# Optimization experiments

Measured on AMD Instinct MI355X. Metric: run time of the kernel, lower is better.

The kernel has to match this reference:

```python
import jax, jax.numpy as jnp
import numpy as np

N_CONV = 3
FEAT = 128
N_RBF = 20
CUTOFF = 5.0
EPS = 1e-15
N_NODES = 10000
N_EDGES = 160000


def setup_inputs() -> dict:
    key = jax.random.key(0)
    ks = jax.random.split(key, 8)
    N, E = N_NODES, N_EDGES
    cg_xyz = jax.random.normal(ks[0], (N, 3), jnp.float32) * 2.0
    # Directed, self-loop-free edge list (both i<j and i>j present, so the
    # original make_directed() is a no-op on this data).
    src = jax.random.randint(ks[1], (E,), 0, N)
    off = jax.random.randint(ks[2], (E,), 1, N)
    CG_nbr_list = jnp.stack([src, (src + off) % N], axis=1)
    cg_s = jax.random.normal(ks[3], (N, FEAT), jnp.float32)
    s = 1.0 / np.sqrt(FEAT)
    # Per-conv-layer weights of ENMessageBlock: inv_dense = Dense(F->F, silu) + Dense(F->3F);
    # dist_embed = ExpNormalBasis(n_rbf) -> Dense(n_rbf->3F) * cosine envelope.
    W1 = jax.random.normal(ks[4], (N_CONV, FEAT, FEAT), jnp.float32) * s
    b1 = jnp.zeros((N_CONV, FEAT), jnp.float32)
    W2 = jax.random.normal(ks[5], (N_CONV, FEAT, 3 * FEAT), jnp.float32) * s
    b2 = jnp.zeros((N_CONV, 3 * FEAT), jnp.float32)
    Wr = jax.random.normal(ks[6], (N_CONV, N_RBF, 3 * FEAT), jnp.float32) / np.sqrt(N_RBF)
    br = jnp.zeros((N_CONV, 3 * FEAT), jnp.float32)
    return {"cg_xyz": cg_xyz, "CG_nbr_list": CG_nbr_list, "cg_s": cg_s,
            "W1": W1, "b1": b1, "W2": W2, "b2": b2, "Wr": Wr, "br": br}


def _expnorm_rbf(dist):
    # ExpNormalBasis: exp(-beta * (exp(-d) - mu)^2), mu in [exp(-cutoff), 1]
    mu = jnp.linspace(np.exp(-CUTOFF), 1.0, N_RBF, dtype=jnp.float32)
    beta = np.float32((2.0 / N_RBF * (1.0 - np.exp(-CUTOFF))) ** -2)
    return jnp.exp(-beta * (jnp.exp(-dist)[:, None] - mu) ** 2)  # (E, n_rbf)


def _cos_envelope(dist):
    return jnp.where(dist < CUTOFF, 0.5 * (jnp.cos(jnp.pi * dist / CUTOFF) + 1.0), 0.0)


def reference(cg_xyz, CG_nbr_list, cg_s, W1, b1, W2, b2, Wr, br):
    N = cg_s.shape[0]
    i, j = CG_nbr_list[:, 0], CG_nbr_list[:, 1]
    r_ij = cg_xyz[j] - cg_xyz[i]                      # (E, 3)
    dist = jnp.sqrt((r_ij ** 2 + EPS).sum(-1))        # (E,)
    unit = r_ij / dist[:, None]                        # (E, 3)
    rbf = _expnorm_rbf(dist)                           # (E, n_rbf) edge-invariant across layers
    env = _cos_envelope(dist)[:, None]                 # (E, 1)

    s_i = cg_s                                         # (N, F)
    v_i = jnp.zeros((N, FEAT, 3), cg_s.dtype)          # (N, F, 3)
    for l in range(N_CONV):
        phi = jax.nn.silu(s_i @ W1[l] + b1[l]) @ W2[l] + b2[l]   # (N, 3F)
        w_s = (rbf @ Wr[l] + br[l]) * env                         # (E, 3F)
        prod = phi[j] * w_s                                       # (E, 3F) gather + gate
        ds = prod[:, :FEAT]                                       # scalar message
        gate_v = prod[:, FEAT:2 * FEAT]                           # gates v_j
        gate_u = prod[:, 2 * FEAT:]                               # gates unit vector
        dv_ij = gate_u[:, :, None] * unit[:, None, :] + gate_v[:, :, None] * v_i[j]  # (E, F, 3)
        s_i = s_i + jax.ops.segment_sum(ds, i, num_segments=N)
        v_i = v_i + jax.ops.segment_sum(dv_ij, i, num_segments=N)
    return s_i, v_i
```

## Files before the change

kernel.cpp:

```cpp
#include <hip/hip_runtime.h>
#include <hip/hip_bf16.h>

#define NRBF 20
#define KAUG 24

typedef __attribute__((ext_vector_type(8))) short short8;
typedef __attribute__((ext_vector_type(4))) float float4v;
typedef __attribute__((ext_vector_type(2))) _Float16 half2v;
typedef unsigned short ushort_t;

__device__ __forceinline__ float bf2f(ushort_t u) {
    return __uint_as_float(((unsigned)u) << 16);
}
__device__ __forceinline__ ushort_t f2bf(float f) {
    unsigned u = __float_as_uint(f);
    u += 0x7FFF + ((u >> 16) & 1);
    return (ushort_t)(u >> 16);
}
__device__ __forceinline__ float ldin(const void* p, size_t idx, int isbf) {
    return isbf ? bf2f(((const ushort_t*)p)[idx]) : ((const float*)p)[idx];
}
__device__ __forceinline__ void stout(void* p, size_t idx, float v, int isbf) {
    if (isbf) ((ushort_t*)p)[idx] = f2bf(v);
    else      ((float*)p)[idx] = v;
}
__device__ __forceinline__ float dot2(half2v a, half2v b, float c) {
#if __has_builtin(__builtin_amdgcn_fdot2)
    return __builtin_amdgcn_fdot2(a, b, c, false);
#else
    return c + (float)a.x * (float)b.x + (float)a.y * (float)b.y;
#endif
}

union F4H {
    float4v f;
    half2v  h[4];
};

__global__ void detect_kernel(const void* __restrict__ xyz, int* __restrict__ flag,
                              int* __restrict__ deg, int N) {
    int idx = blockIdx.x * blockDim.x + threadIdx.x;
    if (idx < N) deg[idx] = 0;
    if (blockIdx.x == 0 && threadIdx.x < 64) {
        const ushort_t* u = (const ushort_t*)xyz;
        unsigned e0 = (u[2 * threadIdx.x] >> 7) & 0xFF;
        unsigned long long bad = __ballot(e0 >= 0x90);
        if (threadIdx.x == 0) *flag = (__popcll(bad) > 2) ? 0 : 1;
    }
}

__global__ void prelude_kernel(const void* __restrict__ xyz, const int* __restrict__ nbr,
                               const void* __restrict__ cg_s,
                               const void* __restrict__ W1, const void* __restrict__ W2,
                               const void* __restrict__ Wr, const void* __restrict__ br,
                               float* __restrict__ s_acc, ushort_t* __restrict__ s_hi,
                               ushort_t* __restrict__ s_lo, int* __restrict__ deg,
                               ushort_t* __restrict__ B1hi, ushort_t* __restrict__ B1lo,
                               ushort_t* __restrict__ B2hi, ushort_t* __restrict__ B2lo,
                               _Float16* __restrict__ WrT,
                               int N128, int E, const int* __restrict__ flagp) {
    int isbf = *flagp;
    int idx = blockIdx.x * blockDim.x + threadIdx.x;
    if (idx < E) {
        int i = nbr[2 * idx], j = nbr[2 * idx + 1];
        float dx = ldin(xyz, 3 * j,     isbf) - ldin(xyz, 3 * i,     isbf);
        float dy = ldin(xyz, 3 * j + 1, isbf) - ldin(xyz, 3 * i + 1, isbf);
        float dz = ldin(xyz, 3 * j + 2, isbf) - ldin(xyz, 3 * i + 2, isbf);
        float dist = sqrtf(dx * dx + dy * dy + dz * dz + 3e-15f);
        if (dist < 5.0f) atomicAdd(&deg[i], 1);
    }
    if (idx < N128) {
        float v = ldin(cg_s, idx, isbf);
        s_acc[idx] = v;
        ushort_t hi = f2bf(v);
        s_hi[idx] = hi;
        s_lo[idx] = f2bf(v - bf2f(hi));
    }
    const int NW1 = 3 * 4 * 8 * 64;
    const int NW2 = 3 * 4 * 24 * 64;
    const int NWT = 3 * 384;
    if (idx < NW1) {
        int lane = idx & 63;
        int t = idx >> 6;
        int nt = t % 8; t /= 8;
        int ks = t % 4; int l = t / 4;
        int n = lane & 15, quad = lane >> 4;
        int col = nt * 16 + n;
        size_t base = (size_t)l * 128 * 128;
        size_t fo = (size_t)idx * 8;
        #pragma unroll
        for (int j = 0; j < 8; j++) {
            int k = ks * 32 + quad * 8 + j;
            float v = ldin(W1, base + (size_t)k * 128 + col, isbf);
            ushort_t hi = f2bf(v);
            B1hi[fo + j] = hi;
            B1lo[fo + j] = f2bf(v - bf2f(hi));
        }
    } else if (idx < NW1 + NW2) {
        int i2 = idx - NW1;
        int lane = i2 & 63;
        int t = i2 >> 6;
        int nt = t % 24; t /= 24;
        int ks = t % 4; int l = t / 4;
        int n = lane & 15, quad = lane >> 4;
        int col = nt * 16 + n;
        size_t base = (size_t)l * 128 * 384;
        size_t fo = (size_t)i2 * 8;
        #pragma unroll
        for (int j = 0; j < 8; j++) {
            int k = ks * 32 + quad * 8 + j;
            float v = ldin(W2, base + (size_t)k * 384 + col, isbf);
            ushort_t hi = f2bf(v);
            B2hi[fo + j] = hi;
            B2lo[fo + j] = f2bf(v - bf2f(hi));
        }
    } else if (idx < NW1 + NW2 + NWT) {
        int i2 = idx - NW1 - NW2;
        int l = i2 / 384, col = i2 % 384;
        _Float16* wt = WrT + ((size_t)l * 384 + col) * KAUG;
        #pragma unroll
        for (int k = 0; k < KAUG; k++) {
            float v = 0.f;
            if (k < NRBF) v = ldin(Wr, ((size_t)l * NRBF + k) * 384 + col, isbf);
            else if (k == NRBF) v = ldin(br, (size_t)l * 384 + col, isbf);
            wt[k] = (_Float16)v;
        }
    }
}

__global__ void scan_kernel(int* __restrict__ deg, int* __restrict__ rowptr, int N) {
    __shared__ int part[256];
    int t = threadIdx.x;
    int chunk = (N + 255) / 256;
    int lo = t * chunk, hi = min(lo + chunk, N);
    int s = 0;
    for (int i = lo; i < hi; i++) s += deg[i];
    part[t] = s;
    __syncthreads();
    for (int off = 1; off < 256; off <<= 1) {
        int v = (t >= off) ? part[t - off] : 0;
        __syncthreads();
        if (t >= off) part[t] += v;
        __syncthreads();
    }
    int base = (t == 0) ? 0 : part[t - 1];
    for (int i = lo; i < hi; i++) {
        rowptr[i] = base;
        int d = deg[i];
        deg[i] = base;
        base += d;
    }
    if (t == 0) rowptr[N] = part[255];
}

__global__ void pack_kernel(const void* __restrict__ xyz, const int* __restrict__ nbr,
                            int* __restrict__ cursor, int* __restrict__ jlist,
                            float4* __restrict__ upos, _Float16* __restrict__ rbfh,
                            int E, const int* __restrict__ flagp) {
    int isbf = *flagp;
    int e = blockIdx.x * blockDim.x + threadIdx.x;
    if (e >= E) return;
    int i = nbr[2 * e], j = nbr[2 * e + 1];
    float dx = ldin(xyz, 3 * j,     isbf) - ldin(xyz, 3 * i,     isbf);
    float dy = ldin(xyz, 3 * j + 1, isbf) - ldin(xyz, 3 * i + 1, isbf);
    float dz = ldin(xyz, 3 * j + 2, isbf) - ldin(xyz, 3 * i + 2, isbf);
    float dist = sqrtf(dx * dx + dy * dy + dz * dz + 3e-15f);
    if (!(dist < 5.0f)) return;
    constexpr float PI = 3.14159265358979323846f;
    float ev = 0.5f * (cosf(PI * dist * 0.2f) + 1.0f);
    int pos = atomicAdd(&cursor[i], 1);
    jlist[pos] = j;
    float inv = 1.0f / dist;
    upos[pos] = make_float4(dx * inv, dy * inv, dz * inv, ev);
    constexpr double EM5 = 0.006737946999085467;
    constexpr float MU0 = (float)EM5;
    constexpr float DMU = (float)((1.0 - EM5) / 19.0);
    constexpr float BETA = (float)(1.0 / ((0.1 * (1.0 - EM5)) * (0.1 * (1.0 - EM5))));
    float ed = expf(-dist);
    _Float16* rp = rbfh + (size_t)pos * KAUG;
    #pragma unroll
    for (int k = 0; k < NRBF; k++) {
        float dmu = ed - (MU0 + k * DMU);
        rp[k] = (_Float16)(ev * expf(-BETA * dmu * dmu));
    }
    rp[NRBF] = (_Float16)ev;
    #pragma unroll
    for (int k = NRBF + 1; k < KAUG; k++) rp[k] = (_Float16)0.f;
}

template <int ACT, int OUTMODE, int NTILES>
__global__ __launch_bounds__(256) void mfma_gemm(
    const ushort_t* __restrict__ Ahi, const ushort_t* __restrict__ Alo,
    const ushort_t* __restrict__ Bhi, const ushort_t* __restrict__ Blo,
    const void* __restrict__ bias, size_t biasoff,
    ushort_t* __restrict__ out_hi, ushort_t* __restrict__ out_lo,
    int M, const int* __restrict__ flagp) {
    constexpr int Ncols = NTILES * 16;
    int isbf = *flagp;
    int nt = blockIdx.x % NTILES;
    int bx = blockIdx.x / NTILES;
    int tid = threadIdx.x;
    int wave = tid >> 6, lane = tid & 63;
    int m = lane & 15, quad = lane >> 4;
    int brow = bx * 64 + wave * 16;
    int row = brow + m;
    float4v acc = {};
    short8 zero8 = {};
    #pragma unroll
    for (int ks = 0; ks < 4; ks++) {
        short8 ah = zero8, al = zero8;
        if (row < M) {
            size_t ao = (size_t)row * 128 + ks * 32 + quad * 8;
            ah = *reinterpret_cast<const short8*>(Ahi + ao);
            al = *reinterpret_cast<const short8*>(Alo + ao);
        }
        size_t fo = (((size_t)ks * NTILES + nt) * 64 + lane) * 8;
        short8 bh = *reinterpret_cast<const short8*>(Bhi + fo);
        acc = __builtin_amdgcn_mfma_f32_16x16x32_bf16(ah, bh, acc, 0, 0, 0);
        acc = __builtin_amdgcn_mfma_f32_16x16x32_bf16(al, bh, acc, 0, 0, 0);
        if (!isbf) {
            short8 bl = *reinterpret_cast<const short8*>(Blo + fo);
            acc = __builtin_amdgcn_mfma_f32_16x16x32_bf16(ah, bl, acc, 0, 0, 0);
        }
    }
    int col = nt * 16 + m;
    float bv = ldin(bias, biasoff + col, isbf);
    #pragma unroll
    for (int r = 0; r < 4; r++) {
        int orow = brow + quad * 4 + r;
        if (orow >= M) continue;
        float x = acc[r] + bv;
        if (ACT) x = x / (1.0f + expf(-x));
        size_t oo = (size_t)orow * Ncols + col;
        ushort_t h = f2bf(x);
        out_hi[oo] = h;
        if (OUTMODE == 0) out_lo[oo] = f2bf(x - bf2f(h));
    }
}

template <int L0, int LAST>
__global__ __launch_bounds__(128, 8) void node_kernel(
    const int* __restrict__ rowptr, const int* __restrict__ jlist,
    const float4* __restrict__ upos, const _Float16* __restrict__ rbfh,
    const _Float16* __restrict__ WrT,
    const ushort_t* __restrict__ phi,
    const float* __restrict__ v_old, const ushort_t* __restrict__ vh_old,
    float* __restrict__ s_acc, ushort_t* __restrict__ s_hi, ushort_t* __restrict__ s_lo,
    float* __restrict__ v_new, ushort_t* __restrict__ vh_new,
    void* __restrict__ out, int N, const int* __restrict__ flagp) {
    int isbf = *flagp;
    int tt = threadIdx.x;
    int node = blockIdx.x;

    F4H wc0[3], wc1[3], wc2[3];
    {
        const float4v* w0p = (const float4v*)(WrT + (size_t)tt * KAUG);
        const float4v* w1p = (const float4v*)(WrT + (size_t)(tt + 128) * KAUG);
        const float4v* w2p = (const float4v*)(WrT + (size_t)(tt + 256) * KAUG);
        #pragma unroll
        for (int r = 0; r < 3; r++) {
            wc0[r].f = w0p[r]; wc1[r].f = w1p[r]; wc2[r].f = w2p[r];
        }
    }
    int start = __builtin_amdgcn_readfirstlane(rowptr[node]);
    int end   = __builtin_amdgcn_readfirstlane(rowptr[node + 1]);

    float dsv = 0.f, ax = 0.f, ay = 0.f, az = 0.f;
    int j = (start < end) ? __builtin_amdgcn_readfirstlane(jlist[start]) : 0;
    for (int k = start; k < end; k++) {
        int jn = j;
        if (k + 1 < end) jn = __builtin_amdgcn_readfirstlane(jlist[k + 1]);
        float4 u4 = upos[k];
        const float4v* rp4 = (const float4v*)(rbfh + (size_t)k * KAUG);
        F4H rv0, rv1, rv2;
        rv0.f = rp4[0]; rv1.f = rp4[1]; rv2.f = rp4[2];
        float w0 = 0.f, w1 = 0.f, w2 = 0.f;
        #pragma unroll
        for (int q = 0; q < 4; q++) {
            w0 = dot2(rv0.h[q], wc0[0].h[q], w0);
            w1 = dot2(rv0.h[q], wc1[0].h[q], w1);
            w2 = dot2(rv0.h[q], wc2[0].h[q], w2);
        }
        #pragma unroll
        for (int q = 0; q < 4; q++) {
            w0 = dot2(rv1.h[q], wc0[1].h[q], w0);
            w1 = dot2(rv1.h[q], wc1[1].h[q], w1);
            w2 = dot2(rv1.h[q], wc2[1].h[q], w2);
        }
        #pragma unroll
        for (int q = 0; q < 4; q++) {
            w0 = dot2(rv2.h[q], wc0[2].h[q], w0);
            w1 = dot2(rv2.h[q], wc1[2].h[q], w1);
            w2 = dot2(rv2.h[q], wc2[2].h[q], w2);
        }
        size_t jb = (size_t)j * 384;
        dsv += bf2f(phi[jb + tt]) * w0;
        float gv = bf2f(phi[jb + 128 + tt]) * w1;
        float gu = bf2f(phi[jb + 256 + tt]) * w2;
        if (L0) {
            ax += gu * u4.x; ay += gu * u4.y; az += gu * u4.z;
        } else {
            const ushort_t* vj = &vh_old[jb + (size_t)tt * 3];
            ax += gu * u4.x + gv * bf2f(vj[0]);
            ay += gu * u4.y + gv * bf2f(vj[1]);
            az += gu * u4.z + gv * bf2f(vj[2]);
        }
        j = jn;
    }
    size_t so = (size_t)node * 128 + tt;
    float snew = s_acc[so] + dsv;
    size_t ib = (size_t)node * 384 + (size_t)tt * 3;
    float vx = L0 ? ax : v_old[ib]     + ax;
    float vy = L0 ? ay : v_old[ib + 1] + ay;
    float vz = L0 ? az : v_old[ib + 2] + az;
    if (LAST) {
        stout(out, so, snew, isbf);
        size_t ob = (size_t)N * 128 + ib;
        stout(out, ob,     vx, isbf);
        stout(out, ob + 1, vy, isbf);
        stout(out, ob + 2, vz, isbf);
    } else {
        s_acc[so] = snew;
        ushort_t hi = f2bf(snew);
        s_hi[so] = hi;
        s_lo[so] = f2bf(snew - bf2f(hi));
        v_new[ib] = vx; v_new[ib + 1] = vy; v_new[ib + 2] = vz;
        vh_new[ib]     = f2bf(vx);
        vh_new[ib + 1] = f2bf(vy);
        vh_new[ib + 2] = f2bf(vz);
    }
}

extern "C" void kernel_launch(void* const* d_in, const int* in_sizes, int n_in,
                              void* d_out, int out_size, void* d_ws, size_t ws_size,
                              hipStream_t stream) {
    const int N = in_sizes[0] / 3;
    const int E = in_sizes[1] / 2;
    const void* xyz  = d_in[0];
    const int*  nbr  = (const int*)d_in[1];
    const void* cg_s = d_in[2];
    const void* W1   = d_in[3];
    const void* b1   = d_in[4];
    const void* W2   = d_in[5];
    const void* b2   = d_in[6];
    const void* Wr   = d_in[7];
    const void* br   = d_in[8];

    size_t off = 0;
    auto alloc = [&](size_t bytes) -> char* {
        char* p = (char*)d_ws + off;
        off = (off + bytes + 63) & ~(size_t)63;
        return p;
    };
    int*       flag   = (int*)alloc(64);
    float*     s_acc  = (float*)alloc((size_t)N * 128 * 4);
    float*     vA     = (float*)alloc((size_t)N * 384 * 4);
    float*     vB     = (float*)alloc((size_t)N * 384 * 4);
    int*       rowptr = (int*)alloc((size_t)(N + 1) * 4);
    int*       deg    = (int*)alloc((size_t)N * 4);
    int*       jlist  = (int*)alloc((size_t)E * 4);
    float4*    upos   = (float4*)alloc((size_t)(E + 16) * 16);
    _Float16*  rbfh   = (_Float16*)alloc((size_t)(E + 16) * KAUG * 2);
    _Float16*  WrT    = (_Float16*)alloc((size_t)3 * 384 * KAUG * 2);
    ushort_t*  s_hi   = (ushort_t*)alloc((size_t)N * 128 * 2);
    ushort_t*  s_lo   = (ushort_t*)alloc((size_t)N * 128 * 2);
    ushort_t*  h_hi   = (ushort_t*)alloc((size_t)N * 128 * 2);
    ushort_t*  h_lo   = (ushort_t*)alloc((size_t)N * 128 * 2);
    ushort_t*  phi    = (ushort_t*)alloc((size_t)N * 384 * 2);
    ushort_t*  vhA    = (ushort_t*)alloc((size_t)N * 384 * 2);
    ushort_t*  vhB    = (ushort_t*)alloc((size_t)N * 384 * 2);
    ushort_t*  B1hi   = (ushort_t*)alloc((size_t)3 * 4 * 8 * 64 * 8 * 2);
    ushort_t*  B1lo   = (ushort_t*)alloc((size_t)3 * 4 * 8 * 64 * 8 * 2);
    ushort_t*  B2hi   = (ushort_t*)alloc((size_t)3 * 4 * 24 * 64 * 8 * 2);
    ushort_t*  B2lo   = (ushort_t*)alloc((size_t)3 * 4 * 24 * 64 * 8 * 2);

    detect_kernel<<<(N + 255) / 256, 256, 0, stream>>>(xyz, flag, deg, N);
    const int N128 = N * 128;
    const int pg = (max(E, N128) + 255) / 256;
    prelude_kernel<<<pg, 256, 0, stream>>>(xyz, nbr, cg_s, W1, W2, Wr, br,
                                           s_acc, s_hi, s_lo, deg,
                                           B1hi, B1lo, B2hi, B2lo, WrT,
                                           N128, E, flag);
    scan_kernel<<<1, 256, 0, stream>>>(deg, rowptr, N);
    pack_kernel<<<(E + 255) / 256, 256, 0, stream>>>(xyz, nbr, deg, jlist, upos,
                                                     rbfh, E, flag);

    const int gx = (N + 63) / 64;
    for (int l = 0; l < 3; l++) {
        mfma_gemm<1, 0, 8><<<gx * 8, 256, 0, stream>>>(
            s_hi, s_lo,
            B1hi + (size_t)l * 4 * 8 * 64 * 8, B1lo + (size_t)l * 4 * 8 * 64 * 8,
            b1, (size_t)l * 128, h_hi, h_lo, N, flag);
        mfma_gemm<0, 1, 24><<<gx * 24, 256, 0, stream>>>(
            h_hi, h_lo,
            B2hi + (size_t)l * 4 * 24 * 64 * 8, B2lo + (size_t)l * 4 * 24 * 64 * 8,
            b2, (size_t)l * 384, phi, (ushort_t*)nullptr, N, flag);
        const _Float16* wrt = WrT + (size_t)l * 384 * KAUG;
        if (l == 0) {
            node_kernel<1, 0><<<N, 128, 0, stream>>>(
                rowptr, jlist, upos, rbfh, wrt, phi,
                vA, vhA, s_acc, s_hi, s_lo, vA, vhA, d_out, N, flag);
        } else if (l == 1) {
            node_kernel<0, 0><<<N, 128, 0, stream>>>(
                rowptr, jlist, upos, rbfh, wrt, phi,
                vA, vhA, s_acc, s_hi, s_lo, vB, vhB, d_out, N, flag);
        } else {
            node_kernel<0, 1><<<N, 128, 0, stream>>>(
                rowptr, jlist, upos, rbfh, wrt, phi,
                vB, vhB, s_acc, s_hi, s_lo, vB, vhB, d_out, N, flag);
        }
    }
}
```

Measured before the change: 329.9 us.

## Fuse all stages into one persistent cooperative kernel with grid syncs

```diff
diff --git a/kernel.cpp b/kernel.cpp
--- a/kernel.cpp
+++ b/kernel.cpp
@@ -1,5 +1,8 @@
 #include <hip/hip_runtime.h>
 #include <hip/hip_bf16.h>
+#include <hip/hip_cooperative_groups.h>
+
+namespace cg = cooperative_groups;
 
 #define NRBF 20
 #define KAUG 24
@@ -37,104 +40,111 @@
     half2v  h[4];
 };
 
-__global__ void detect_kernel(const void* __restrict__ xyz, int* __restrict__ flag,
-                              int* __restrict__ deg, int N) {
-    int idx = blockIdx.x * blockDim.x + threadIdx.x;
-    if (idx < N) deg[idx] = 0;
-    if (blockIdx.x == 0 && threadIdx.x < 64) {
-        const ushort_t* u = (const ushort_t*)xyz;
-        unsigned e0 = (u[2 * threadIdx.x] >> 7) & 0xFF;
+struct KParams {
+    const void* xyz; const int* nbr; const void* cg_s;
+    const void* W1;  const void* b1; const void* W2; const void* b2;
+    const void* Wr;  const void* br;
+    int* flag; float* s_acc; float* vA; float* vB;
+    int* rowptr; int* deg; int* jlist; float4* upos;
+    _Float16* rbfh; _Float16* WrT;
+    ushort_t* s_hi; ushort_t* s_lo; ushort_t* h_hi; ushort_t* h_lo;
+    ushort_t* phi;  ushort_t* vhA;  ushort_t* vhB;
+    ushort_t* B1hi; ushort_t* B1lo; ushort_t* B2hi; ushort_t* B2lo;
+    void* out; int N, E, gx;
+};
+
+__device__ __forceinline__ void phase_detect(const KParams& p) {
+    int tid = threadIdx.x;
+    for (int idx = blockIdx.x * 256 + tid; idx < p.N; idx += gridDim.x * 256)
+        p.deg[idx] = 0;
+    if (blockIdx.x == 0 && tid < 64) {
+        const ushort_t* u = (const ushort_t*)p.xyz;
+        unsigned e0 = (u[2 * tid] >> 7) & 0xFF;
         unsigned long long bad = __ballot(e0 >= 0x90);
-        if (threadIdx.x == 0) *flag = (__popcll(bad) > 2) ? 0 : 1;
-    }
-}
-
-__global__ void prelude_kernel(const void* __restrict__ xyz, const int* __restrict__ nbr,
-                               const void* __restrict__ cg_s,
-                               const void* __restrict__ W1, const void* __restrict__ W2,
-                               const void* __restrict__ Wr, const void* __restrict__ br,
-                               float* __restrict__ s_acc, ushort_t* __restrict__ s_hi,
-                               ushort_t* __restrict__ s_lo, int* __restrict__ deg,
-                               ushort_t* __restrict__ B1hi, ushort_t* __restrict__ B1lo,
-                               ushort_t* __restrict__ B2hi, ushort_t* __restrict__ B2lo,
-                               _Float16* __restrict__ WrT,
-                               int N128, int E, const int* __restrict__ flagp) {
-    int isbf = *flagp;
-    int idx = blockIdx.x * blockDim.x + threadIdx.x;
-    if (idx < E) {
-        int i = nbr[2 * idx], j = nbr[2 * idx + 1];
-        float dx = ldin(xyz, 3 * j,     isbf) - ldin(xyz, 3 * i,     isbf);
-        float dy = ldin(xyz, 3 * j + 1, isbf) - ldin(xyz, 3 * i + 1, isbf);
-        float dz = ldin(xyz, 3 * j + 2, isbf) - ldin(xyz, 3 * i + 2, isbf);
-        float dist = sqrtf(dx * dx + dy * dy + dz * dz + 3e-15f);
-        if (dist < 5.0f) atomicAdd(&deg[i], 1);
-    }
-    if (idx < N128) {
-        float v = ldin(cg_s, idx, isbf);
-        s_acc[idx] = v;
-        ushort_t hi = f2bf(v);
-        s_hi[idx] = hi;
-        s_lo[idx] = f2bf(v - bf2f(hi));
-    }
+        if (tid == 0) *p.flag = (__popcll(bad) > 2) ? 0 : 1;
+    }
+}
+
+__device__ void phase_prelude(const KParams& p, int isbf) {
+    const int N128 = p.N * 128;
     const int NW1 = 3 * 4 * 8 * 64;
     const int NW2 = 3 * 4 * 24 * 64;
     const int NWT = 3 * 384;
-    if (idx < NW1) {
-        int lane = idx & 63;
-        int t = idx >> 6;
-        int nt = t % 8; t /= 8;
-        int ks = t % 4; int l = t / 4;
-        int n = lane & 15, quad = lane >> 4;
-        int col = nt * 16 + n;
-        size_t base = (size_t)l * 128 * 128;
-        size_t fo = (size_t)idx * 8;
-        #pragma unroll
-        for (int j = 0; j < 8; j++) {
-            int k = ks * 32 + quad * 8 + j;
-            float v = ldin(W1, base + (size_t)k * 128 + col, isbf);
+    int tot = (N128 > p.E) ? N128 : p.E;
+    for (int idx = blockIdx.x * 256 + threadIdx.x; idx < tot; idx += gridDim.x * 256) {
+        if (idx < p.E) {
+            int i = p.nbr[2 * idx], j = p.nbr[2 * idx + 1];
+            float dx = ldin(p.xyz, 3 * j,     isbf) - ldin(p.xyz, 3 * i,     isbf);
+            float dy = ldin(p.xyz, 3 * j + 1, isbf) - ldin(p.xyz, 3 * i + 1, isbf);
+            float dz = ldin(p.xyz, 3 * j + 2, isbf) - ldin(p.xyz, 3 * i + 2, isbf);
+            float dist = sqrtf(dx * dx + dy * dy + dz * dz + 3e-15f);
+            if (dist < 5.0f) atomicAdd(&p.deg[i], 1);
+        }
+        if (idx < N128) {
+            float v = ldin(p.cg_s, idx, isbf);
+            p.s_acc[idx] = v;
             ushort_t hi = f2bf(v);
-            B1hi[fo + j] = hi;
-            B1lo[fo + j] = f2bf(v - bf2f(hi));
-        }
-    } else if (idx < NW1 + NW2) {
-        int i2 = idx - NW1;
-        int lane = i2 & 63;
-        int t = i2 >> 6;
-        int nt = t % 24; t /= 24;
-        int ks = t % 4; int l = t / 4;
-        int n = lane & 15, quad = lane >> 4;
-        int col = nt * 16 + n;
-        size_t base = (size_t)l * 128 * 384;
-        size_t fo = (size_t)i2 * 8;
-        #pragma unroll
-        for (int j = 0; j < 8; j++) {
-            int k = ks * 32 + quad * 8 + j;
-            float v = ldin(W2, base + (size_t)k * 384 + col, isbf);
-            ushort_t hi = f2bf(v);
-            B2hi[fo + j] = hi;
-            B2lo[fo + j] = f2bf(v - bf2f(hi));
-        }
-    } else if (idx < NW1 + NW2 + NWT) {
-        int i2 = idx - NW1 - NW2;
-        int l = i2 / 384, col = i2 % 384;
-        _Float16* wt = WrT + ((size_t)l * 384 + col) * KAUG;
-        #pragma unroll
-        for (int k = 0; k < KAUG; k++) {
-            float v = 0.f;
-            if (k < NRBF) v = ldin(Wr, ((size_t)l * NRBF + k) * 384 + col, isbf);
-            else if (k == NRBF) v = ldin(br, (size_t)l * 384 + col, isbf);
-            wt[k] = (_Float16)v;
-        }
-    }
-}
-
-__global__ void scan_kernel(int* __restrict__ deg, int* __restrict__ rowptr, int N) {
+            p.s_hi[idx] = hi;
+            p.s_lo[idx] = f2bf(v - bf2f(hi));
+        }
+        if (idx < NW1) {
+            int lane = idx & 63;
+            int t = idx >> 6;
+            int nt = t % 8; t /= 8;
+            int ks = t % 4; int l = t / 4;
+            int n = lane & 15, quad = lane >> 4;
+            int col = nt * 16 + n;
+            size_t base = (size_t)l * 128 * 128;
+            size_t fo = (size_t)idx * 8;
+            #pragma unroll
+            for (int j = 0; j < 8; j++) {
+                int k = ks * 32 + quad * 8 + j;
+                float v = ldin(p.W1, base + (size_t)k * 128 + col, isbf);
+                ushort_t hi = f2bf(v);
+                p.B1hi[fo + j] = hi;
+                p.B1lo[fo + j] = f2bf(v - bf2f(hi));
+            }
+        } else if (idx < NW1 + NW2) {
+            int i2 = idx - NW1;
+            int lane = i2 & 63;
+            int t = i2 >> 6;
+            int nt = t % 24; t /= 24;
+            int ks = t % 4; int l = t / 4;
+            int n = lane & 15, quad = lane >> 4;
+            int col = nt * 16 + n;
+            size_t base = (size_t)l * 128 * 384;
+            size_t fo = (size_t)i2 * 8;
+            #pragma unroll
+            for (int j = 0; j < 8; j++) {
+                int k = ks * 32 + quad * 8 + j;
+                float v = ldin(p.W2, base + (size_t)k * 384 + col, isbf);
+                ushort_t hi = f2bf(v);
+                p.B2hi[fo + j] = hi;
+                p.B2lo[fo + j] = f2bf(v - bf2f(hi));
+            }
+        } else if (idx < NW1 + NW2 + NWT) {
+            int i2 = idx - NW1 - NW2;
+            int l = i2 / 384, col = i2 % 384;
+            _Float16* wt = p.WrT + ((size_t)l * 384 + col) * KAUG;
+            #pragma unroll
+            for (int k = 0; k < KAUG; k++) {
+                float v = 0.f;
+                if (k < NRBF) v = ldin(p.Wr, ((size_t)l * NRBF + k) * 384 + col, isbf);
+                else if (k == NRBF) v = ldin(p.br, (size_t)l * 384 + col, isbf);
+                wt[k] = (_Float16)v;
+            }
+        }
+    }
+}
+
+__device__ void scan_block(const KParams& p) {
     __shared__ int part[256];
     int t = threadIdx.x;
+    int N = p.N;
     int chunk = (N + 255) / 256;
     int lo = t * chunk, hi = min(lo + chunk, N);
     int s = 0;
-    for (int i = lo; i < hi; i++) s += deg[i];
+    for (int i = lo; i < hi; i++) s += p.deg[i];
     part[t] = s;
     __syncthreads();
     for (int off = 1; off < 256; off <<= 1) {
@@ -145,39 +155,34 @@
     }
     int base = (t == 0) ? 0 : part[t - 1];
     for (int i = lo; i < hi; i++) {
-        rowptr[i] = base;
-        int d = deg[i];
-        deg[i] = base;
+        p.rowptr[i] = base;
+        int d = p.deg[i];
+        p.deg[i] = base;
         base += d;
     }
-    if (t == 0) rowptr[N] = part[255];
-}
-
-__global__ void pack_kernel(const void* __restrict__ xyz, const int* __restrict__ nbr,
-                            int* __restrict__ cursor, int* __restrict__ jlist,
-                            float4* __restrict__ upos, _Float16* __restrict__ rbfh,
-                            int E, const int* __restrict__ flagp) {
-    int isbf = *flagp;
-    int e = blockIdx.x * blockDim.x + threadIdx.x;
-    if (e >= E) return;
-    int i = nbr[2 * e], j = nbr[2 * e + 1];
-    float dx = ldin(xyz, 3 * j,     isbf) - ldin(xyz, 3 * i,     isbf);
-    float dy = ldin(xyz, 3 * j + 1, isbf) - ldin(xyz, 3 * i + 1, isbf);
-    float dz = ldin(xyz, 3 * j + 2, isbf) - ldin(xyz, 3 * i + 2, isbf);
+    if (t == 0) p.rowptr[N] = part[255];
+}
+
+__device__ void pack_edge(const KParams& p, int isbf, int e) {
+    if (e >= p.E) return;
+    int i = p.nbr[2 * e], j = p.nbr[2 * e + 1];
+    float dx = ldin(p.xyz, 3 * j,     isbf) - ldin(p.xyz, 3 * i,     isbf);
+    float dy = ldin(p.xyz, 3 * j + 1, isbf) - ldin(p.xyz, 3 * i + 1, isbf);
+    float dz = ldin(p.xyz, 3 * j + 2, isbf) - ldin(p.xyz, 3 * i + 2, isbf);
     float dist = sqrtf(dx * dx + dy * dy + dz * dz + 3e-15f);
     if (!(dist < 5.0f)) return;
     constexpr float PI = 3.14159265358979323846f;
     float ev = 0.5f * (cosf(PI * dist * 0.2f) + 1.0f);
-    int pos = atomicAdd(&cursor[i], 1);
-    jlist[pos] = j;
+    int pos = atomicAdd(&p.deg[i], 1);
+    p.jlist[pos] = j;
     float inv = 1.0f / dist;
-    upos[pos] = make_float4(dx * inv, dy * inv, dz * inv, ev);
+    p.upos[pos] = make_float4(dx * inv, dy * inv, dz * inv, ev);
     constexpr double EM5 = 0.006737946999085467;
     constexpr float MU0 = (float)EM5;
     constexpr float DMU = (float)((1.0 - EM5) / 19.0);
     constexpr float BETA = (float)(1.0 / ((0.1 * (1.0 - EM5)) * (0.1 * (1.0 - EM5))));
     float ed = expf(-dist);
-    _Float16* rp = rbfh + (size_t)pos * KAUG;
+    _Float16* rp = p.rbfh + (size_t)pos * KAUG;
     #pragma unroll
     for (int k = 0; k < NRBF; k++) {
         float dmu = ed - (MU0 + k * DMU);
@@ -189,16 +194,15 @@
 }
 
 template <int ACT, int OUTMODE, int NTILES>
-__global__ __launch_bounds__(256) void mfma_gemm(
-    const ushort_t* __restrict__ Ahi, const ushort_t* __restrict__ Alo,
+__device__ __forceinline__ void gemm_item(
+    int item, const ushort_t* __restrict__ Ahi, const ushort_t* __restrict__ Alo,
     const ushort_t* __restrict__ Bhi, const ushort_t* __restrict__ Blo,
     const void* __restrict__ bias, size_t biasoff,
     ushort_t* __restrict__ out_hi, ushort_t* __restrict__ out_lo,
-    int M, const int* __restrict__ flagp) {
+    int M, int isbf) {
     constexpr int Ncols = NTILES * 16;
-    int isbf = *flagp;
-    int nt = blockIdx.x % NTILES;
-    int bx = blockIdx.x / NTILES;
+    int nt = item % NTILES;
+    int bx = item / NTILES;
     int tid = threadIdx.x;
     int wave = tid >> 6, lane = tid & 63;
     int m = lane & 15, quad = lane >> 4;
@@ -238,97 +242,159 @@
     }
 }
 
+__device__ void phase_g1(const KParams& p, int isbf, int l, bool withScan) {
+    const ushort_t* Bh = p.B1hi + (size_t)l * 4 * 8 * 64 * 8;
+    const ushort_t* Bl = p.B1lo + (size_t)l * 4 * 8 * 64 * 8;
+    size_t boff = (size_t)l * 128;
+    int g1 = p.gx * 8;
+    int items = g1 + (withScan ? 1 : 0);
+    for (int it = blockIdx.x; it < items; it += gridDim.x) {
+        if (withScan) {
+            if (it == 0) { scan_block(p); continue; }
+            gemm_item<1, 0, 8>(it - 1, p.s_hi, p.s_lo, Bh, Bl, p.b1, boff,
+                               p.h_hi, p.h_lo, p.N, isbf);
+        } else {
+            gemm_item<1, 0, 8>(it, p.s_hi, p.s_lo, Bh, Bl, p.b1, boff,
+                               p.h_hi, p.h_lo, p.N, isbf);
+        }
+    }
+}
+
+__device__ void phase_g2(const KParams& p, int isbf, int l, bool withPack) {
+    const ushort_t* Bh = p.B2hi + (size_t)l * 4 * 24 * 64 * 8;
+    const ushort_t* Bl = p.B2lo + (size_t)l * 4 * 24 * 64 * 8;
+    size_t boff = (size_t)l * 384;
+    int g2 = p.gx * 24;
+    int packItems = withPack ? (p.E + 255) / 256 : 0;
+    int items = g2 + packItems;
+    for (int it = blockIdx.x; it < items; it += gridDim.x) {
+        if (it < g2) {
+            gemm_item<0, 1, 24>(it, p.h_hi, p.h_lo, Bh, Bl, p.b2, boff,
+                                p.phi, (ushort_t*)nullptr, p.N, isbf);
+        } else {
+            pack_edge(p, isbf, (it - g2) * 256 + threadIdx.x);
+        }
+    }
+}
+
 template <int L0, int LAST>
-__global__ __launch_bounds__(128, 8) void node_kernel(
-    const int* __restrict__ rowptr, const int* __restrict__ jlist,
-    const float4* __restrict__ upos, const _Float16* __restrict__ rbfh,
-    const _Float16* __restrict__ WrT,
-    const ushort_t* __restrict__ phi,
-    const float* __restrict__ v_old, const ushort_t* __restrict__ vh_old,
-    float* __restrict__ s_acc, ushort_t* __restrict__ s_hi, ushort_t* __restrict__ s_lo,
-    float* __restrict__ v_new, ushort_t* __restrict__ vh_new,
-    void* __restrict__ out, int N, const int* __restrict__ flagp) {
-    int isbf = *flagp;
-    int tt = threadIdx.x;
-    int node = blockIdx.x;
+__device__ void phase_node(const KParams& p, int isbf, const _Float16* WrTl,
+                           const float* v_old, const ushort_t* vh_old,
+                           float* v_new, ushort_t* vh_new) {
+    int tid = threadIdx.x;
+    int half = tid >> 7;
+    int tt = tid & 127;
 
     F4H wc0[3], wc1[3], wc2[3];
     {
-        const float4v* w0p = (const float4v*)(WrT + (size_t)tt * KAUG);
-        const float4v* w1p = (const float4v*)(WrT + (size_t)(tt + 128) * KAUG);
-        const float4v* w2p = (const float4v*)(WrT + (size_t)(tt + 256) * KAUG);
+        const float4v* w0p = (const float4v*)(WrTl + (size_t)tt * KAUG);
+        const float4v* w1p = (const float4v*)(WrTl + (size_t)(tt + 128) * KAUG);
+        const float4v* w2p = (const float4v*)(WrTl + (size_t)(tt + 256) * KAUG);
         #pragma unroll
         for (int r = 0; r < 3; r++) {
             wc0[r].f = w0p[r]; wc1[r].f = w1p[r]; wc2[r].f = w2p[r];
         }
     }
-    int start = __builtin_amdgcn_readfirstlane(rowptr[node]);
-    int end   = __builtin_amdgcn_readfirstlane(rowptr[node + 1]);
-
-    float dsv = 0.f, ax = 0.f, ay = 0.f, az = 0.f;
-    int j = (start < end) ? __builtin_amdgcn_readfirstlane(jlist[start]) : 0;
-    for (int k = start; k < end; k++) {
-        int jn = j;
-        if (k + 1 < end) jn = __builtin_amdgcn_readfirstlane(jlist[k + 1]);
-        float4 u4 = upos[k];
-        const float4v* rp4 = (const float4v*)(rbfh + (size_t)k * KAUG);
-        F4H rv0, rv1, rv2;
-        rv0.f = rp4[0]; rv1.f = rp4[1]; rv2.f = rp4[2];
-        float w0 = 0.f, w1 = 0.f, w2 = 0.f;
-        #pragma unroll
-        for (int q = 0; q < 4; q++) {
-            w0 = dot2(rv0.h[q], wc0[0].h[q], w0);
-            w1 = dot2(rv0.h[q], wc1[0].h[q], w1);
-            w2 = dot2(rv0.h[q], wc2[0].h[q], w2);
-        }
-        #pragma unroll
-        for (int q = 0; q < 4; q++) {
-            w0 = dot2(rv1.h[q], wc0[1].h[q], w0);
-            w1 = dot2(rv1.h[q], wc1[1].h[q], w1);
-            w2 = dot2(rv1.h[q], wc2[1].h[q], w2);
-        }
-        #pragma unroll
-        for (int q = 0; q < 4; q++) {
-            w0 = dot2(rv2.h[q], wc0[2].h[q], w0);
-            w1 = dot2(rv2.h[q], wc1[2].h[q], w1);
-            w2 = dot2(rv2.h[q], wc2[2].h[q], w2);
-        }
-        size_t jb = (size_t)j * 384;
-        dsv += bf2f(phi[jb + tt]) * w0;
-        float gv = bf2f(phi[jb + 128 + tt]) * w1;
-        float gu = bf2f(phi[jb + 256 + tt]) * w2;
-        if (L0) {
-            ax += gu * u4.x; ay += gu * u4.y; az += gu * u4.z;
+    int items = (p.N + 1) >> 1;
+    for (int it = blockIdx.x; it < items; it += gridDim.x) {
+        int node = it * 2 + half;
+        if (node >= p.N) continue;
+        int start = __builtin_amdgcn_readfirstlane(p.rowptr[node]);
+        int end   = __builtin_amdgcn_readfirstlane(p.rowptr[node + 1]);
+
+        float dsv = 0.f, ax = 0.f, ay = 0.f, az = 0.f;
+        int j = (start < end) ? __builtin_amdgcn_readfirstlane(p.jlist[start]) : 0;
+        for (int k = start; k < end; k++) {
+            int jn = j;
+            if (k + 1 < end) jn = __builtin_amdgcn_readfirstlane(p.jlist[k + 1]);
+            float4 u4 = p.upos[k];
+            const float4v* rp4 = (const float4v*)(p.rbfh + (size_t)k * KAUG);
+            F4H rv0, rv1, rv2;
+            rv0.f = rp4[0]; rv1.f = rp4[1]; rv2.f = rp4[2];
+            float w0 = 0.f, w1 = 0.f, w2 = 0.f;
+            #pragma unroll
+            for (int q = 0; q < 4; q++) {
+                w0 = dot2(rv0.h[q], wc0[0].h[q], w0);
+                w1 = dot2(rv0.h[q], wc1[0].h[q], w1);
+                w2 = dot2(rv0.h[q], wc2[0].h[q], w2);
+            }
+            #pragma unroll
+            for (int q = 0; q < 4; q++) {
+                w0 = dot2(rv1.h[q], wc0[1].h[q], w0);
+                w1 = dot2(rv1.h[q], wc1[1].h[q], w1);
+                w2 = dot2(rv1.h[q], wc2[1].h[q], w2);
+            }
+            #pragma unroll
+            for (int q = 0; q < 4; q++) {
+                w0 = dot2(rv2.h[q], wc0[2].h[q], w0);
+                w1 = dot2(rv2.h[q], wc1[2].h[q], w1);
+                w2 = dot2(rv2.h[q], wc2[2].h[q], w2);
+            }
+            size_t jb = (size_t)j * 384;
+            dsv += bf2f(p.phi[jb + tt]) * w0;
+            float gv = bf2f(p.phi[jb + 128 + tt]) * w1;
+            float gu = bf2f(p.phi[jb + 256 + tt]) * w2;
+            if (L0) {
+                ax += gu * u4.x; ay += gu * u4.y; az += gu * u4.z;
+            } else {
+                const ushort_t* vj = &vh_old[jb + (size_t)tt * 3];
+                ax += gu * u4.x + gv * bf2f(vj[0]);
+                ay += gu * u4.y + gv * bf2f(vj[1]);
+                az += gu * u4.z + gv * bf2f(vj[2]);
+            }
+            j = jn;
+        }
+        size_t so = (size_t)node * 128 + tt;
+        float snew = p.s_acc[so] + dsv;
+        size_t ib = (size_t)node * 384 + (size_t)tt * 3;
+        float vx = L0 ? ax : v_old[ib]     + ax;
+        float vy = L0 ? ay : v_old[ib + 1] + ay;
+        float vz = L0 ? az : v_old[ib + 2] + az;
+        if (LAST) {
+            stout(p.out, so, snew, isbf);
+            size_t ob = (size_t)p.N * 128 + ib;
+            stout(p.out, ob,     vx, isbf);
+            stout(p.out, ob + 1, vy, isbf);
+            stout(p.out, ob + 2, vz, isbf);
         } else {
-            const ushort_t* vj = &vh_old[jb + (size_t)tt * 3];
-            ax += gu * u4.x + gv * bf2f(vj[0]);
-            ay += gu * u4.y + gv * bf2f(vj[1]);
-            az += gu * u4.z + gv * bf2f(vj[2]);
-        }
-        j = jn;
-    }
-    size_t so = (size_t)node * 128 + tt;
-    float snew = s_acc[so] + dsv;
-    size_t ib = (size_t)node * 384 + (size_t)tt * 3;
-    float vx = L0 ? ax : v_old[ib]     + ax;
-    float vy = L0 ? ay : v_old[ib + 1] + ay;
-    float vz = L0 ? az : v_old[ib + 2] + az;
-    if (LAST) {
-        stout(out, so, snew, isbf);
-        size_t ob = (size_t)N * 128 + ib;
-        stout(out, ob,     vx, isbf);
-        stout(out, ob + 1, vy, isbf);
-        stout(out, ob + 2, vz, isbf);
-    } else {
-        s_acc[so] = snew;
-        ushort_t hi = f2bf(snew);
-        s_hi[so] = hi;
-        s_lo[so] = f2bf(snew - bf2f(hi));
-        v_new[ib] = vx; v_new[ib + 1] = vy; v_new[ib + 2] = vz;
-        vh_new[ib]     = f2bf(vx);
-        vh_new[ib + 1] = f2bf(vy);
-        vh_new[ib + 2] = f2bf(vz);
-    }
+            p.s_acc[so] = snew;
+            ushort_t hi = f2bf(snew);
+            p.s_hi[so] = hi;
+            p.s_lo[so] = f2bf(snew - bf2f(hi));
+            v_new[ib] = vx; v_new[ib + 1] = vy; v_new[ib + 2] = vz;
+            vh_new[ib]     = f2bf(vx);
+            vh_new[ib + 1] = f2bf(vy);
+            vh_new[ib + 2] = f2bf(vz);
+        }
+    }
+}
+
+__global__ __launch_bounds__(256, 4) void mega_kernel(KParams p) {
+    cg::grid_group grid = cg::this_grid();
+
+    phase_detect(p);
+    grid.sync();
+    int isbf = *p.flag;
+    phase_prelude(p, isbf);
+    grid.sync();
+
+    phase_g1(p, isbf, 0, true);
+    grid.sync();
+    phase_g2(p, isbf, 0, true);
+    grid.sync();
+    phase_node<1, 0>(p, isbf, p.WrT, p.vA, p.vhA, p.vA, p.vhA);
+    grid.sync();
+    phase_g1(p, isbf, 1, false);
+    grid.sync();
+    phase_g2(p, isbf, 1, false);
+    grid.sync();
+    phase_node<0, 0>(p, isbf, p.WrT + (size_t)384 * KAUG, p.vA, p.vhA, p.vB, p.vhB);
+    grid.sync();
+    phase_g1(p, isbf, 2, false);
+    grid.sync();
+    phase_g2(p, isbf, 2, false);
+    grid.sync();
+    phase_node<0, 1>(p, isbf, p.WrT + (size_t)2 * 384 * KAUG, p.vB, p.vhB, p.vB, p.vhB);
 }
 
 extern "C" void kernel_launch(void* const* d_in, const int* in_sizes, int n_in,
@@ -336,15 +402,6 @@
                               hipStream_t stream) {
     const int N = in_sizes[0] / 3;
     const int E = in_sizes[1] / 2;
-    const void* xyz  = d_in[0];
-    const int*  nbr  = (const int*)d_in[1];
-    const void* cg_s = d_in[2];
-    const void* W1   = d_in[3];
-    const void* b1   = d_in[4];
-    const void* W2   = d_in[5];
-    const void* b2   = d_in[6];
-    const void* Wr   = d_in[7];
-    const void* br   = d_in[8];
 
     size_t off = 0;
     auto alloc = [&](size_t bytes) -> char* {
@@ -352,62 +409,57 @@
         off = (off + bytes + 63) & ~(size_t)63;
         return p;
     };
-    int*       flag   = (int*)alloc(64);
-    float*     s_acc  = (float*)alloc((size_t)N * 128 * 4);
-    float*     vA     = (float*)alloc((size_t)N * 384 * 4);
-    float*     vB     = (float*)alloc((size_t)N * 384 * 4);
-    int*       rowptr = (int*)alloc((size_t)(N + 1) * 4);
-    int*       deg    = (int*)alloc((size_t)N * 4);
-    int*       jlist  = (int*)alloc((size_t)E * 4);
-    float4*    upos   = (float4*)alloc((size_t)(E + 16) * 16);
-    _Float16*  rbfh   = (_Float16*)alloc((size_t)(E + 16) * KAUG * 2);
-    _Float16*  WrT    = (_Float16*)alloc((size_t)3 * 384 * KAUG * 2);
-    ushort_t*  s_hi   = (ushort_t*)alloc((size_t)N * 128 * 2);
-    ushort_t*  s_lo   = (ushort_t*)alloc((size_t)N * 128 * 2);
-    ushort_t*  h_hi   = (ushort_t*)alloc((size_t)N * 128 * 2);
-    ushort_t*  h_lo   = (ushort_t*)alloc((size_t)N * 128 * 2);
-    ushort_t*  phi    = (ushort_t*)alloc((size_t)N * 384 * 2);
-    ushort_t*  vhA    = (ushort_t*)alloc((size_t)N * 384 * 2);
-    ushort_t*  vhB    = (ushort_t*)alloc((size_t)N * 384 * 2);
-    ushort_t*  B1hi   = (ushort_t*)alloc((size_t)3 * 4 * 8 * 64 * 8 * 2);
-    ushort_t*  B1lo   = (ushort_t*)alloc((size_t)3 * 4 * 8 * 64 * 8 * 2);
-    ushort_t*  B2hi   = (ushort_t*)alloc((size_t)3 * 4 * 24 * 64 * 8 * 2);
-    ushort_t*  B2lo   = (ushort_t*)alloc((size_t)3 * 4 * 24 * 64 * 8 * 2);
-
-    detect_kernel<<<(N + 255) / 256, 256, 0, stream>>>(xyz, flag, deg, N);
-    const int N128 = N * 128;
-    const int pg = (max(E, N128) + 255) / 256;
-    prelude_kernel<<<pg, 256, 0, stream>>>(xyz, nbr, cg_s, W1, W2, Wr, br,
-                                           s_acc, s_hi, s_lo, deg,
-                                           B1hi, B1lo, B2hi, B2lo, WrT,
-                                           N128, E, flag);
-    scan_kernel<<<1, 256, 0, stream>>>(deg, rowptr, N);
-    pack_kernel<<<(E + 255) / 256, 256, 0, stream>>>(xyz, nbr, deg, jlist, upos,
-                                                     rbfh, E, flag);
-
-    const int gx = (N + 63) / 64;
-    for (int l = 0; l < 3; l++) {
-        mfma_gemm<1, 0, 8><<<gx * 8, 256, 0, stream>>>(
-            s_hi, s_lo,
-            B1hi + (size_t)l * 4 * 8 * 64 * 8, B1lo + (size_t)l * 4 * 8 * 64 * 8,
-            b1, (size_t)l * 128, h_hi, h_lo, N, flag);
-        mfma_gemm<0, 1, 24><<<gx * 24, 256, 0, stream>>>(
-            h_hi, h_lo,
-            B2hi + (size_t)l * 4 * 24 * 64 * 8, B2lo + (size_t)l * 4 * 24 * 64 * 8,
-            b2, (size_t)l * 384, phi, (ushort_t*)nullptr, N, flag);
-        const _Float16* wrt = WrT + (size_t)l * 384 * KAUG;
-        if (l == 0) {
-            node_kernel<1, 0><<<N, 128, 0, stream>>>(
-                rowptr, jlist, upos, rbfh, wrt, phi,
-                vA, vhA, s_acc, s_hi, s_lo, vA, vhA, d_out, N, flag);
-        } else if (l == 1) {
-            node_kernel<0, 0><<<N, 128, 0, stream>>>(
-                rowptr, jlist, upos, rbfh, wrt, phi,
-                vA, vhA, s_acc, s_hi, s_lo, vB, vhB, d_out, N, flag);
-        } else {
-            node_kernel<0, 1><<<N, 128, 0, stream>>>(
-                rowptr, jlist, upos, rbfh, wrt, phi,
-                vB, vhB, s_acc, s_hi, s_lo, vB, vhB, d_out, N, flag);
-        }
-    }
-}
+    KParams P;
+    P.xyz  = d_in[0];
+    P.nbr  = (const int*)d_in[1];
+    P.cg_s = d_in[2];
+    P.W1   = d_in[3];
+    P.b1   = d_in[4];
+    P.W2   = d_in[5];
+    P.b2   = d_in[6];
+    P.Wr   = d_in[7];
+    P.br   = d_in[8];
+    P.flag   = (int*)alloc(64);
+    P.s_acc  = (float*)alloc((size_t)N * 128 * 4);
+    P.vA     = (float*)alloc((size_t)N * 384 * 4);
+    P.vB     = (float*)alloc((size_t)N * 384 * 4);
+    P.rowptr = (int*)alloc((size_t)(N + 1) * 4);
+    P.deg    = (int*)alloc((size_t)N * 4);
+    P.jlist  = (int*)alloc((size_t)E * 4);
+    P.upos   = (float4*)alloc((size_t)(E + 16) * 16);
+    P.rbfh   = (_Float16*)alloc((size_t)(E + 16) * KAUG * 2);
+    P.WrT    = (_Float16*)alloc((size_t)3 * 384 * KAUG * 2);
+    P.s_hi   = (ushort_t*)alloc((size_t)N * 128 * 2);
+    P.s_lo   = (ushort_t*)alloc((size_t)N * 128 * 2);
+    P.h_hi   = (ushort_t*)alloc((size_t)N * 128 * 2);
+    P.h_lo   = (ushort_t*)alloc((size_t)N * 128 * 2);
+    P.phi    = (ushort_t*)alloc((size_t)N * 384 * 2);
+    P.vhA    = (ushort_t*)alloc((size_t)N * 384 * 2);
+    P.vhB    = (ushort_t*)alloc((size_t)N * 384 * 2);
+    P.B1hi   = (ushort_t*)alloc((size_t)3 * 4 * 8 * 64 * 8 * 2);
+    P.B1lo   = (ushort_t*)alloc((size_t)3 * 4 * 8 * 64 * 8 * 2);
+    P.B2hi   = (ushort_t*)alloc((size_t)3 * 4 * 24 * 64 * 8 * 2);
+    P.B2lo   = (ushort_t*)alloc((size_t)3 * 4 * 24 * 64 * 8 * 2);
+    P.out = d_out;
+    P.N = N;
+    P.E = E;
+    P.gx = (N + 63) / 64;
+
+    static int coopGrid = 0;
+    if (coopGrid == 0) {
+        int bpc = 0;
+        if (hipOccupancyMaxActiveBlocksPerMultiprocessor(&bpc, mega_kernel, 256, 0)
+                != hipSuccess || bpc < 1)
+            bpc = 1;
+        if (bpc > 8) bpc = 8;
+        hipDeviceProp_t prop{};
+        int dev = 0;
+        hipGetDevice(&dev);
+        int cus = (hipGetDeviceProperties(&prop, dev) == hipSuccess &&
+                   prop.multiProcessorCount > 0) ? prop.multiProcessorCount : 256;
+        coopGrid = bpc * cus;
+    }
+
+    void* args[] = { (void*)&P };
+    hipLaunchCooperativeKernel(mega_kernel, dim3(coopGrid), dim3(256), args, 0, stream);
+}
```

New measurement: 1.137 ms. 245% more time.
